# Kernel optimization log

Measured on AMD Instinct MI355X. Metric: run time of the kernel, lower is better.

## Reference

```python
import jax, jax.numpy as jnp
import numpy as np

NUM_CHANNELS = 32
NUM_GRIDS = 2048
BATCH = 32
MIN_XI = 0.1
MAX_XI = 5.0
DX = 0.08


def setup_inputs() -> dict:
    key = jax.random.key(0)
    k1, k2 = jax.random.split(key)
    inputs = jax.random.normal(k1, (BATCH, NUM_GRIDS), dtype=jnp.float32)
    # uniform real-space grid, centered at 0, spacing DX
    grids = (jnp.arange(NUM_GRIDS, dtype=jnp.float32) - NUM_GRIDS / 2) * DX
    # eta initialized ~ N(0, 1e-4) as in the original RandomNormal(0, 0.0001)
    eta = 0.0001 * jax.random.normal(k2, (NUM_CHANNELS,), dtype=jnp.float32)
    return {"inputs": inputs, "grids": grids, "eta": eta}


def reference(inputs, grids, eta):
    # widths in (MIN_XI, MAX_XI) via sigmoid reparameterization, shape (C,)
    widths = MIN_XI + (MAX_XI - MIN_XI) * jax.nn.sigmoid(eta)
    # pairwise displacements |x_n - x_m|, shape (N, N)
    absdisp = jnp.abs(grids[:, None] - grids[None, :])
    # exponential (Laplace) kernels, shape (N, N, C)
    kernels = jnp.exp(-absdisp[:, :, None] / widths) / (2.0 * widths)
    # tensordot(inputs, kernels, axes=(1, 0)) -> (B, N, C), scaled by dx
    return jnp.einsum("bn,nmc->bmc", inputs, kernels) * DX
```

## Files before the change

kernel.cpp:

```cpp
#include <hip/hip_runtime.h>
#include <math.h>

namespace {

constexpr int NCH   = 32;
constexpr int NG    = 2048;
constexpr int BATCH = 32;
constexpr float DXC = 0.08f;

constexpr int NSEG   = 8;
constexpr int SEGLEN = NG / NSEG;
constexpr int NCHUNK = 32;
constexpr int CHL    = NG / NCHUNK;
constexpr int NSUB   = 8;
constexpr int SUBL   = CHL / NSUB;
constexpr int CPS    = NCHUNK / NSEG;

__global__ __launch_bounds__(1024)
void egc_kernel(const float* __restrict__ inputs,
                const float* __restrict__ eta,
                float* __restrict__ out) {
    __shared__ float xs[NG];
    __shared__ float pw[64][NCH];
    __shared__ float F8[CPS][NSUB][NCH];
    __shared__ float G8[CPS][NSUB][NCH];
    __shared__ float Ef[NCHUNK][NCH];
    __shared__ float Eb[NCHUNK][NCH];
    __shared__ float CF[NCHUNK][NCH];
    __shared__ float CB[NCHUNK][NCH];

    const int tid = threadIdx.x;
    const int c   = tid & 31;
    const int t   = tid >> 5;
    const int b   = blockIdx.x >> 3;
    const int seg = blockIdx.x & (NSEG - 1);

    const float e   = eta[c];
    const float sig = 1.0f / (1.0f + expf(-e));
    const float w   = 0.1f + 4.9f * sig;
    const float lam = DXC / w;
    const float s   = 0.5f * DXC / w;

    const float* xrow = inputs + (size_t)b * NG;
    xs[tid]        = xrow[tid];
    xs[tid + 1024] = xrow[tid + 1024];
    pw[t][c]      = expf(-lam * (float)t);
    pw[t + 32][c] = expf(-lam * (float)(t + 32));
    __syncthreads();

    float p[SUBL];
#pragma unroll
    for (int i = 0; i < SUBL; ++i) p[i] = pw[i][c];
    const float r  = p[1];
    const float p8 = pw[SUBL][c];

    {
        const int base = t * CHL;
        float sf[NSUB], sb[NSUB];
#pragma unroll
        for (int ss = 0; ss < NSUB; ++ss) {
            const int o = base + ss * SUBL;
            float xv[SUBL];
#pragma unroll
            for (int i = 0; i < SUBL; ++i) xv[i] = xs[o + i];
            float f = 0.0f, g = 0.0f;
#pragma unroll
            for (int i = 0; i < SUBL; ++i) {
                f = fmaf(p[SUBL - 1 - i], xv[i], f);
                g = fmaf(p[i],            xv[i], g);
            }
            sf[ss] = f; sb[ss] = g;
        }

        const int  tc  = t - seg * CPS;
        const bool own = (tc >= 0) && (tc < CPS);
        float fa = 0.0f;
#pragma unroll
        for (int ss = 0; ss < NSUB; ++ss) {
            fa = fmaf(p8, fa, sf[ss]);
            if (own) F8[tc][ss][c] = fa;
        }
        float ga = 0.0f;
#pragma unroll
        for (int ss = NSUB - 1; ss >= 0; --ss) {
            ga = fmaf(p8, ga, sb[ss]);
            if (own) G8[tc][ss][c] = ga;
        }
        Ef[t][c] = fa;
        Eb[t][c] = ga;
    }
    __syncthreads();

    {
        const float rho = expf(-lam * (float)CHL);
        if (t == 0) {
            float ev[NCHUNK];
#pragma unroll
            for (int k = 0; k < NCHUNK; ++k) ev[k] = Ef[k][c];
            float fe = 0.0f;
#pragma unroll
            for (int k = 0; k < NCHUNK; ++k) { CF[k][c] = fe; fe = fmaf(rho, fe, ev[k]); }
        } else if (t == 2) {
            float ev[NCHUNK];
#pragma unroll
            for (int k = 0; k < NCHUNK; ++k) ev[k] = Eb[k][c];
            float ge = 0.0f;
#pragma unroll
            for (int k = NCHUNK - 1; k >= 0; --k) { CB[k][c] = ge; ge = fmaf(rho, ge, ev[k]); }
        }
    }
    __syncthreads();

    const int T     = seg * (SEGLEN / SUBL) + t;
    const int chunk = T >> 3;
    const int sub   = T & (NSUB - 1);
    const int tc    = chunk - seg * CPS;
    const int m0    = T * SUBL;

    float fin = CF[chunk][c] * pw[SUBL * sub][c];
    if (sub > 0) fin += F8[tc][sub - 1][c];
    float gin;
    if (sub < NSUB - 1)
        gin = G8[tc][sub + 1][c] + CB[chunk][c] * pw[CHL - SUBL * (sub + 1)][c];
    else
        gin = CB[chunk][c];

    float xv[SUBL], Fv[SUBL];
#pragma unroll
    for (int i = 0; i < SUBL; ++i) xv[i] = xs[m0 + i];

    float f = fin;
#pragma unroll
    for (int i = 0; i < SUBL; ++i) { f = fmaf(r, f, xv[i]); Fv[i] = f; }

    float g = gin;
    float* orow = out + ((size_t)b * NG + m0) * NCH + c;
#pragma unroll
    for (int i = SUBL - 1; i >= 0; --i) {
        g = fmaf(r, g, xv[i]);
        orow[(size_t)i * NCH] = s * (Fv[i] + g - xv[i]);
    }
}

}

extern "C" void kernel_launch(void* const* d_in, const int* in_sizes, int n_in,
                              void* d_out, int out_size, void* d_ws, size_t ws_size,
                              hipStream_t stream) {
    const float* inputs = (const float*)d_in[0];
    const float* eta    = (const float*)d_in[2];
    float* out          = (float*)d_out;

    dim3 grid(BATCH * NSEG);
    dim3 block(1024);
    hipLaunchKernelGGL(egc_kernel, grid, block, 0, stream, inputs, eta, out);
}
```

Baseline: 62.09 us.

## Split each batch row into 16 segments with 512-thread blocks

Doubles the number of segments per batch row and halves the block size to 512 threads, so each thread now computes the chunk prefix sums for two chunks. Inputs are loaded as float4, and rho comes from squaring a cached power instead of calling expf. The aim is more blocks and better occupancy (launch bounds allow 4 blocks per CU). The cost is that every block still redundantly computes the chunk scans for the whole row.

New measurement: 63.02 us. About the same (+1.5%).

```diff
diff --git a/kernel.cpp b/kernel.cpp
--- a/kernel.cpp
+++ b/kernel.cpp
@@ -8,15 +8,16 @@
 constexpr int BATCH = 32;
 constexpr float DXC = 0.08f;
 
-constexpr int NSEG   = 8;
+constexpr int NSEG   = 16;
 constexpr int SEGLEN = NG / NSEG;
 constexpr int NCHUNK = 32;
 constexpr int CHL    = NG / NCHUNK;
 constexpr int NSUB   = 8;
 constexpr int SUBL   = CHL / NSUB;
 constexpr int CPS    = NCHUNK / NSEG;
+constexpr int NT     = 16;
 
-__global__ __launch_bounds__(1024)
+__global__ __launch_bounds__(512, 4)
 void egc_kernel(const float* __restrict__ inputs,
                 const float* __restrict__ eta,
                 float* __restrict__ out) {
@@ -32,20 +33,20 @@
     const int tid = threadIdx.x;
     const int c   = tid & 31;
     const int t   = tid >> 5;
-    const int b   = blockIdx.x >> 3;
+    const int b   = blockIdx.x >> 4;
     const int seg = blockIdx.x & (NSEG - 1);
 
     const float e   = eta[c];
-    const float sig = 1.0f / (1.0f + expf(-e));
-    const float w   = 0.1f + 4.9f * sig;
+    const float w   = 0.1f + 4.9f / (1.0f + expf(-e));
     const float lam = DXC / w;
     const float s   = 0.5f * DXC / w;
 
     const float* xrow = inputs + (size_t)b * NG;
-    xs[tid]        = xrow[tid];
-    xs[tid + 1024] = xrow[tid + 1024];
+    reinterpret_cast<float4*>(xs)[tid] = reinterpret_cast<const float4*>(xrow)[tid];
     pw[t][c]      = expf(-lam * (float)t);
+    pw[t + 16][c] = expf(-lam * (float)(t + 16));
     pw[t + 32][c] = expf(-lam * (float)(t + 32));
+    pw[t + 48][c] = expf(-lam * (float)(t + 48));
     __syncthreads();
 
     float p[SUBL];
@@ -54,8 +55,10 @@
     const float r  = p[1];
     const float p8 = pw[SUBL][c];
 
-    {
-        const int base = t * CHL;
+    const bool own = (t == seg);
+#pragma unroll
+    for (int kk = 0; kk < CPS; ++kk) {
+        const int base = (2 * t + kk) * CHL;
         float sf[NSUB], sb[NSUB];
 #pragma unroll
         for (int ss = 0; ss < NSUB; ++ss) {
@@ -71,28 +74,26 @@
             }
             sf[ss] = f; sb[ss] = g;
         }
-
-        const int  tc  = t - seg * CPS;
-        const bool own = (tc >= 0) && (tc < CPS);
         float fa = 0.0f;
 #pragma unroll
         for (int ss = 0; ss < NSUB; ++ss) {
             fa = fmaf(p8, fa, sf[ss]);
-            if (own) F8[tc][ss][c] = fa;
+            if (own) F8[kk][ss][c] = fa;
         }
         float ga = 0.0f;
 #pragma unroll
         for (int ss = NSUB - 1; ss >= 0; --ss) {
             ga = fmaf(p8, ga, sb[ss]);
-            if (own) G8[tc][ss][c] = ga;
+            if (own) G8[kk][ss][c] = ga;
         }
-        Ef[t][c] = fa;
-        Eb[t][c] = ga;
+        Ef[2 * t + kk][c] = fa;
+        Eb[2 * t + kk][c] = ga;
     }
     __syncthreads();
 
     {
-        const float rho = expf(-lam * (float)CHL);
+        const float p32 = pw[32][c];
+        const float rho = p32 * p32;
         if (t == 0) {
             float ev[NCHUNK];
 #pragma unroll
@@ -111,17 +112,17 @@
     }
     __syncthreads();
 
-    const int T     = seg * (SEGLEN / SUBL) + t;
+    const int T     = seg * NT + t;
     const int chunk = T >> 3;
     const int sub   = T & (NSUB - 1);
-    const int tc    = chunk - seg * CPS;
+    const int tc    = t >> 3;
     const int m0    = T * SUBL;
 
     float fin = CF[chunk][c] * pw[SUBL * sub][c];
     if (sub > 0) fin += F8[tc][sub - 1][c];
     float gin;
     if (sub < NSUB - 1)
-        gin = G8[tc][sub + 1][c] + CB[chunk][c] * pw[CHL - SUBL * (sub + 1)][c];
+        gin = fmaf(CB[chunk][c], pw[CHL - SUBL * (sub + 1)][c], G8[tc][sub + 1][c]);
     else
         gin = CB[chunk][c];
 
@@ -152,6 +153,6 @@
     float* out          = (float*)d_out;
 
     dim3 grid(BATCH * NSEG);
-    dim3 block(1024);
+    dim3 block(512);
     hipLaunchKernelGGL(egc_kernel, grid, block, 0, stream, inputs, eta, out);
 }
```
